# Performance work log

Measured on AMD Instinct MI355X. Metric: run time of the kernel, lower is better.

The kernel has to match this reference:

```python
import jax, jax.numpy as jnp
import numpy as np

N_NODES = 50000
N_EDGES = 600000
IN_DIM = 128
HID = 128


def gcn_conv(x, W, b, src, dst, num_nodes):
    """PyG-style GCNConv: add self-loops, symmetric D^-1/2 (A+I) D^-1/2 normalization."""
    xw = x @ W  # [N, H]
    loop = jnp.arange(num_nodes)
    s = jnp.concatenate([src, loop])
    d = jnp.concatenate([dst, loop])
    deg = jax.ops.segment_sum(jnp.ones_like(d, dtype=xw.dtype), d, num_segments=num_nodes)
    dinv = jax.lax.rsqrt(deg)  # deg >= 1 thanks to self-loops
    norm = dinv[s] * dinv[d]  # [E+N]
    msgs = xw[s] * norm[:, None]  # gather + scale, [E+N, H]
    out = jax.ops.segment_sum(msgs, d, num_segments=num_nodes)
    return out + b


def setup_inputs() -> dict:
    key = jax.random.key(0)
    ks = jax.random.split(key, 12)
    sc_in = 1.0 / np.sqrt(IN_DIM)
    sc_h = 1.0 / np.sqrt(HID)
    sc_2h = 1.0 / np.sqrt(2 * HID)
    return {
        "x": jax.random.normal(ks[0], (N_NODES, IN_DIM), jnp.float32),
        "hidden_state": jax.random.normal(ks[1], (N_NODES, HID), jnp.float32),
        "edge_index": jax.random.randint(ks[2], (2, N_EDGES), 0, N_NODES, dtype=jnp.int32),
        "W_in": jax.random.normal(ks[3], (IN_DIM, HID), jnp.float32) * sc_in,
        "b_in": jnp.zeros((HID,), jnp.float32),
        "W_hid": jax.random.normal(ks[4], (HID, HID), jnp.float32) * sc_h,
        "b_hid": jnp.zeros((HID,), jnp.float32),
        "W_z": jax.random.normal(ks[5], (2 * HID, HID), jnp.float32) * sc_2h,
        "b_z": jnp.zeros((HID,), jnp.float32),
        "W_r": jax.random.normal(ks[6], (2 * HID, HID), jnp.float32) * sc_2h,
        "b_r": jnp.zeros((HID,), jnp.float32),
        "W_c": jax.random.normal(ks[7], (2 * HID, HID), jnp.float32) * sc_2h,
        "b_c": jnp.zeros((HID,), jnp.float32),
    }


def reference(x, hidden_state, edge_index, W_in, b_in, W_hid, b_hid, W_z, b_z, W_r, b_r, W_c, b_c):
    src, dst = edge_index[0], edge_index[1]
    n = x.shape[0]
    # two stacked GCN layers (dropout identity in eval mode)
    h1 = jax.nn.relu(gcn_conv(x, W_in, b_in, src, dst, n))
    emb = gcn_conv(h1, W_hid, b_hid, src, dst, n)  # [N, H]
    # GRU-style gating
    combined = jnp.concatenate([emb, hidden_state], axis=1)  # [N, 2H]
    update = jax.nn.sigmoid(combined @ W_z + b_z)
    reset = jax.nn.sigmoid(combined @ W_r + b_r)
    cand_in = jnp.concatenate([emb, reset * hidden_state], axis=1)
    candidate = jnp.tanh(cand_in @ W_c + b_c)
    new_hidden = (1.0 - update) * hidden_state + update * candidate
    return new_hidden
```

## Files before the change

kernel.cpp:

```cpp
#include <hip/hip_runtime.h>
#include <cstdint>
#include <cstddef>

typedef unsigned short u16;
typedef unsigned int   u32;

typedef __bf16 bf8   __attribute__((ext_vector_type(8)));
typedef float  f32x4 __attribute__((ext_vector_type(4)));

__device__ __forceinline__ float b2f(u16 v) {
  union { u32 i; float f; } c; c.i = ((u32)v) << 16; return c.f;
}
__device__ __forceinline__ u16 f2b(float f) {
  union { u32 i; float f; } c; c.f = f;
  u32 x = c.i;
  u32 r = (x + 0x7FFFu + ((x >> 16) & 1u)) >> 16;
  return (u16)r;
}
__device__ __forceinline__ float sigf(float x) { return 1.0f / (1.0f + __expf(-x)); }
__device__ __forceinline__ float tanhfast(float x) { return 2.0f * sigf(2.0f * x) - 1.0f; }

__device__ __forceinline__ bf8 cvt8(const float* __restrict__ p) {
  f32x4 lo = *(const f32x4*)p;
  f32x4 hi = *(const f32x4*)(p + 4);
  union { u16 s[8]; bf8 v; } c;
#pragma unroll
  for (int i = 0; i < 4; ++i) { c.s[i] = f2b(lo[i]); c.s[4 + i] = f2b(hi[i]); }
  return c.v;
}

__device__ __forceinline__ void ld_lds16(const u16* g, u16* l) {
  __builtin_amdgcn_global_load_lds((const __attribute__((address_space(1))) void*)g,
                                   (__attribute__((address_space(3))) void*)l, 16, 0, 0);
}

#define CSR_STRIDE 80

__global__ __launch_bounds__(256) void k_transpose(
    const float* __restrict__ W0, const float* __restrict__ W1,
    const float* __restrict__ W2, const float* __restrict__ W3,
    const float* __restrict__ W4,
    u16* __restrict__ B0, u16* __restrict__ B1, u16* __restrict__ B2,
    u16* __restrict__ B3, u16* __restrict__ B4,
    int* __restrict__ cnt, int N) {
  if (blockIdx.x >= 64) {
    int i = (blockIdx.x - 64) * 256 + threadIdx.x;
    if (i < N) cnt[i] = 0;
    return;
  }
  int t = blockIdx.x * 256 + threadIdx.x;
  const float* in; u16* out; int f;
  if (t < 2048)       { in = W0; out = B0; f = t; }
  else if (t < 4096)  { in = W1; out = B1; f = t - 2048; }
  else if (t < 8192)  { in = W2; out = B2; f = t - 4096; }
  else if (t < 12288) { in = W3; out = B3; f = t - 8192; }
  else                { in = W4; out = B4; f = t - 12288; }
  int ln = f & 15, quad = (f >> 4) & 3, c = (f >> 6) & 7, ks = (f >> 9) & 3, hh = f >> 11;
  int n = c * 16 + ln;
  int k0 = hh * 128 + ks * 32 + quad * 8;
  union { u16 s[8]; uint4 q; } tmp;
#pragma unroll
  for (int j = 0; j < 8; ++j) tmp.s[j] = f2b(in[(size_t)(k0 + j) * 128 + n]);
  *(uint4*)(out + (size_t)f * 8) = tmp.q;
}

__global__ void k_fill(const int* __restrict__ src, const int* __restrict__ dst,
                       int* __restrict__ cnt, int* __restrict__ csr, int E) {
  int e = blockIdx.x * 256 + threadIdx.x;
  if (e < E) {
    int d = dst[e];
    int pos = atomicAdd(&cnt[d], 1);
    if (pos < CSR_STRIDE) csr[(size_t)d * CSR_STRIDE + pos] = src[e];
  }
}

__global__ __launch_bounds__(256) void k_agg(const u16* __restrict__ y,
                                             const int* __restrict__ cnt,
                                             const int* __restrict__ csr,
                                             const float* __restrict__ bias,
                                             u16* __restrict__ out, int relu, int N) {
  int wv = (blockIdx.x * 256 + threadIdx.x) >> 6;
  int lane = threadIdx.x & 63;
  if (wv >= N) return;
  int g = lane >> 4, t = lane & 15;
  const uint4* yq = (const uint4*)y;
  int deg = cnt[wv];
  int degc = (deg < 64) ? deg : 64;
  long base = (long)wv * CSR_STRIDE;
  int myidx = (lane < degc) ? csr[base + lane] : 0;

  float a[8];
#pragma unroll
  for (int j = 0; j < 8; ++j) a[j] = 0.0f;

  for (int b = 0; b < degc; b += 8) {
    int e0 = b + g, e1 = b + 4 + g;
    int s0 = __shfl(myidx, (e0 < degc) ? e0 : 0, 64);
    int s1 = __shfl(myidx, (e1 < degc) ? e1 : 0, 64);
    uint4 v0 = yq[(size_t)s0 * 16 + t];
    uint4 v1 = yq[(size_t)s1 * 16 + t];
    if (e0 < degc) {
      const u32* w = (const u32*)&v0;
#pragma unroll
      for (int i = 0; i < 4; ++i) { a[2*i] += b2f((u16)(w[i] & 0xFFFF)); a[2*i+1] += b2f((u16)(w[i] >> 16)); }
    }
    if (e1 < degc) {
      const u32* w = (const u32*)&v1;
#pragma unroll
      for (int i = 0; i < 4; ++i) { a[2*i] += b2f((u16)(w[i] & 0xFFFF)); a[2*i+1] += b2f((u16)(w[i] >> 16)); }
    }
  }
#pragma unroll
  for (int j = 0; j < 8; ++j) {
    a[j] += __shfl_xor(a[j], 16, 64);
    a[j] += __shfl_xor(a[j], 32, 64);
  }
  if (g == 0) {
    int degt = (deg < CSR_STRIDE) ? deg : CSR_STRIDE;
    for (int p = 64; p < degt; ++p) {
      int s = csr[base + p];
      uint4 v = yq[(size_t)s * 16 + t];
      const u32* w = (const u32*)&v;
#pragma unroll
      for (int i = 0; i < 4; ++i) { a[2*i] += b2f((u16)(w[i] & 0xFFFF)); a[2*i+1] += b2f((u16)(w[i] >> 16)); }
    }
    uint4 sv = yq[(size_t)wv * 16 + t];
    const u32* w = (const u32*)&sv;
#pragma unroll
    for (int i = 0; i < 4; ++i) { a[2*i] += b2f((u16)(w[i] & 0xFFFF)); a[2*i+1] += b2f((u16)(w[i] >> 16)); }
    float di = rsqrtf((float)deg + 1.0f);
    f32x4 b0 = *(const f32x4*)(bias + t * 8);
    f32x4 b1 = *(const f32x4*)(bias + t * 8 + 4);
    union { u16 s[8]; uint4 q; } o;
#pragma unroll
    for (int j = 0; j < 8; ++j) {
      float r = di * a[j] + ((j < 4) ? b0[j] : b1[j - 4]);
      if (relu) r = fmaxf(r, 0.0f);
      o.s[j] = f2b(r);
    }
    ((uint4*)out)[(size_t)wv * 16 + t] = o.q;
  }
}

template <bool AF>
__global__ __launch_bounds__(256) void k_gemm(
    const void* __restrict__ Av,
    const u16* __restrict__ Bt,
    const int* __restrict__ cnt,
    u16* __restrict__ outb, int M) {
  __shared__ __align__(16) u16 bs[16384];
  int tid = threadIdx.x;
  int lane = tid & 63, wave = tid >> 6;
  int ln = lane & 15, quad = lane >> 4;
  int rowbase = blockIdx.x * 64 + wave * 16;
  int rowA = rowbase + ln;
  long rA = (rowA < M) ? rowA : (M - 1);

  {
    const u16* g = Bt + wave * 4096 + lane * 8;
    u16* l = bs + wave * 4096;
#pragma unroll
    for (int i = 0; i < 8; ++i) ld_lds16(g + i * 512, l + i * 512);
  }

  bf8 af[4];
#pragma unroll
  for (int ks = 0; ks < 4; ++ks) {
    int kk = ks * 32 + quad * 8;
    if (AF) af[ks] = cvt8((const float*)Av + rA * 128 + kk);
    else    af[ks] = *(const bf8*)((const u16*)Av + rA * 128 + kk);
  }

  f32x4 acc[8];
#pragma unroll
  for (int c = 0; c < 8; ++c) { acc[c][0] = 0.f; acc[c][1] = 0.f; acc[c][2] = 0.f; acc[c][3] = 0.f; }

  __syncthreads();
#pragma unroll
  for (int ks = 0; ks < 4; ++ks) {
#pragma unroll
    for (int c = 0; c < 8; ++c) {
      bf8 bfr = *(const bf8*)(bs + ks * 4096 + c * 512 + lane * 8);
      acc[c] = __builtin_amdgcn_mfma_f32_16x16x32_bf16(af[ks], bfr, acc[c], 0, 0, 0);
    }
  }

  int rb = rowbase + quad * 4;
  float rs[4];
#pragma unroll
  for (int r = 0; r < 4; ++r) {
    int row = rb + r;
    rs[r] = (row < M) ? rsqrtf((float)cnt[row] + 1.0f) : 0.0f;
  }
#pragma unroll
  for (int c = 0; c < 8; ++c) {
    int col = c * 16 + ln;
#pragma unroll
    for (int r = 0; r < 4; ++r) {
      int row = rb + r;
      if (row < M) outb[(size_t)row * 128 + col] = f2b(acc[c][r] * rs[r]);
    }
  }
}

__global__ __launch_bounds__(256, 2) void k_gru(
    const u16* __restrict__ emb, const float* __restrict__ h,
    const u16* __restrict__ Btz, const u16* __restrict__ Btr, const u16* __restrict__ Btc,
    const float* __restrict__ bz, const float* __restrict__ br, const float* __restrict__ bc,
    float* __restrict__ out, int M) {
  __shared__ __align__(16) u16 lds[20480];
  int tid = threadIdx.x;
  int lane = tid & 63, wave = tid >> 6;
  int ln = lane & 15, quad = lane >> 4;
  int rowbase = blockIdx.x * 64 + wave * 16;
  int rowA = rowbase + ln;
  long rA = (rowA < M) ? rowA : (M - 1);
  int rb = rowbase + quad * 4;
  u16* const atw = lds + 12288 + wave * 2048;

  auto stage_zr = [&](int t, int s) {
    const u16* src = ((t & 1) ? Btr : Btz) + (t >> 1) * 4096;
#pragma unroll
    for (int i = 0; i < 2; ++i) {
      int off = (wave * 2 + i) * 512;
      ld_lds16(src + off + lane * 8, &lds[s * 4096 + off]);
    }
  };
  auto stage_c = [&](int k, int s) {
#pragma unroll
    for (int i = 0; i < 2; ++i) {
      int off = (wave * 2 + i) * 512;
      ld_lds16(Btc + k * 4096 + off + lane * 8, &lds[s * 4096 + off]);
    }
  };

  bf8 af_e[4], af_h[4];
#pragma unroll
  for (int ks = 0; ks < 4; ++ks)
    af_e[ks] = *(const bf8*)(emb + rA * 128 + ks * 32 + quad * 8);
#pragma unroll
  for (int ks = 0; ks < 4; ++ks)
    af_h[ks] = cvt8(h + rA * 128 + ks * 32 + quad * 8);

  stage_zr(0, 0);
  stage_zr(1, 1);

  f32x4 accz[8], accr[8];
#pragma unroll
  for (int c = 0; c < 8; ++c) {
    accz[c][0] = 0.f; accz[c][1] = 0.f; accz[c][2] = 0.f; accz[c][3] = 0.f;
    accr[c][0] = 0.f; accr[c][1] = 0.f; accr[c][2] = 0.f; accr[c][3] = 0.f;
  }

#pragma unroll
  for (int t = 0; t < 16; ++t) {
    if (t < 15) asm volatile("s_waitcnt vmcnt(2)\n\ts_barrier" ::: "memory");
    else        asm volatile("s_waitcnt vmcnt(0)\n\ts_barrier" ::: "memory");
    if (t < 14) stage_zr(t + 2, (t + 2) % 3);
    int ks = t >> 1;
    bf8 af = (ks < 4) ? af_e[ks] : af_h[ks - 4];
    int s = t % 3;
    f32x4* acc = (t & 1) ? accr : accz;
#pragma unroll
    for (int c = 0; c < 8; ++c) {
      bf8 bfr = *(const bf8*)(&lds[s * 4096 + (c * 64 + lane) * 8]);
      acc[c] = __builtin_amdgcn_mfma_f32_16x16x32_bf16(af, bfr, acc[c], 0, 0, 0);
    }
  }

  stage_c(0, 1);
  stage_c(1, 2);

  f32x4 hc[8];
#pragma unroll
  for (int c = 0; c < 8; ++c) {
    int col = c * 16 + ln;
#pragma unroll
    for (int r = 0; r < 4; ++r) {
      int row = rb + r;
      hc[c][r] = (row < M) ? h[(size_t)row * 128 + col] : 0.0f;
    }
  }

#pragma unroll
  for (int c = 0; c < 8; ++c) {
    int col = c * 16 + ln;
    float bzc = bz[col], brc = br[col];
#pragma unroll
    for (int r = 0; r < 4; ++r) {
      float uu = sigf(accz[c][r] + bzc);
      float rr = sigf(accr[c][r] + brc);
      accz[c][r] = uu;
      int wl = quad * 4 + r;
      int idx = (wl * 128 + col) ^ ((wl & 7) << 3);
      atw[idx] = f2b(rr * hc[c][r]);
      accr[c][r] = 0.0f;
    }
  }
  bf8 af_at[4];
#pragma unroll
  for (int ks = 0; ks < 4; ++ks) {
    int wl = ln;
    int idx = (wl * 128 + ks * 32 + quad * 8) ^ ((wl & 7) << 3);
    af_at[ks] = *(const bf8*)(&atw[idx]);
  }

#pragma unroll
  for (int j = 0; j < 8; ++j) {
    if (j < 7) asm volatile("s_waitcnt vmcnt(2)\n\ts_barrier" ::: "memory");
    else       asm volatile("s_waitcnt vmcnt(0)\n\ts_barrier" ::: "memory");
    if (j < 6) stage_c(j + 2, j % 3);
    bf8 af = (j < 4) ? af_e[j] : af_at[j - 4];
    int s = (j + 1) % 3;
#pragma unroll
    for (int c = 0; c < 8; ++c) {
      bf8 bfr = *(const bf8*)(&lds[s * 4096 + (c * 64 + lane) * 8]);
      accr[c] = __builtin_amdgcn_mfma_f32_16x16x32_bf16(af, bfr, accr[c], 0, 0, 0);
    }
  }

#pragma unroll
  for (int c = 0; c < 8; ++c) {
    int col = c * 16 + ln;
    float bcc = bc[col];
#pragma unroll
    for (int r = 0; r < 4; ++r) {
      int row = rb + r;
      if (row < M) {
        float cd = tanhfast(accr[c][r] + bcc);
        float uu = accz[c][r];
        out[(size_t)row * 128 + col] = (1.0f - uu) * hc[c][r] + uu * cd;
      }
    }
  }
}

extern "C" void kernel_launch(void* const* d_in, const int* in_sizes, int n_in,
                              void* d_out, int out_size, void* d_ws, size_t ws_size,
                              hipStream_t stream) {
  const float* x     = (const float*)d_in[0];
  const float* h     = (const float*)d_in[1];
  const int*   ei    = (const int*)d_in[2];
  const float* W_in  = (const float*)d_in[3];
  const float* b_in  = (const float*)d_in[4];
  const float* W_hid = (const float*)d_in[5];
  const float* b_hid = (const float*)d_in[6];
  const float* W_z   = (const float*)d_in[7];
  const float* b_z   = (const float*)d_in[8];
  const float* W_r   = (const float*)d_in[9];
  const float* b_r   = (const float*)d_in[10];
  const float* W_c   = (const float*)d_in[11];
  const float* b_c   = (const float*)d_in[12];

  const int N = in_sizes[0] / 128;
  const int E = in_sizes[2] / 2;
  const int* src = ei;
  const int* dst = ei + E;

  char* p = (char*)d_ws;
  auto carve = [&](size_t bytes) { char* r = p; p += (bytes + 255) & ~(size_t)255; return r; };
  u16* Bt_in   = (u16*)carve((size_t)16384 * 2);
  u16* Bt_hid  = (u16*)carve((size_t)16384 * 2);
  u16* Bt_z    = (u16*)carve((size_t)32768 * 2);
  u16* Bt_r    = (u16*)carve((size_t)32768 * 2);
  u16* Bt_c    = (u16*)carve((size_t)32768 * 2);
  int* cnt  = (int*)carve((size_t)N * 4);
  int* csr  = (int*)carve((size_t)N * CSR_STRIDE * 4);
  u16* y    = (u16*)carve((size_t)N * 128 * 2);
  u16* h1   = (u16*)carve((size_t)N * 128 * 2);
  u16* emb  = (u16*)carve((size_t)N * 128 * 2);

  int gN = (N + 255) / 256;
  int gE = (E + 255) / 256;
  int gG = (N + 63) / 64;
  int gA = (N + 3) / 4;

  k_transpose<<<64 + gN, 256, 0, stream>>>(W_in, W_hid, W_z, W_r, W_c,
                                           Bt_in, Bt_hid, Bt_z, Bt_r, Bt_c, cnt, N);
  k_fill<<<gE, 256, 0, stream>>>(src, dst, cnt, csr, E);

  k_gemm<true><<<gG, 256, 0, stream>>>(x, Bt_in, cnt, y, N);
  k_agg<<<gA, 256, 0, stream>>>(y, cnt, csr, b_in, h1, 1, N);
  k_gemm<false><<<gG, 256, 0, stream>>>(h1, Bt_hid, cnt, y, N);
  k_agg<<<gA, 256, 0, stream>>>(y, cnt, csr, b_hid, emb, 0, N);
  k_gru<<<gG, 256, 0, stream>>>(emb, h, Bt_z, Bt_r, Bt_c, b_z, b_r, b_c, (float*)d_out, N);
}
```

Before: 255.7 us.

## Restructure GRU kernel to single-wave blocks with barrier-free double-buffered staging

Turns the GRU gating kernel from 4-wave blocks, which shared each staged weight tile through a triple-buffered LDS ring with s_barrier, into one-wave blocks of 16 rows. Each wave stages the whole weight tile itself into a double buffer, using vmcnt and lgkmcnt waits instead of workgroup barriers. This removes barrier stalls and halves LDS per block, which should allow more resident blocks. In exchange, every 16-row block reloads the full weight matrices, so L2 traffic for weights is four times higher, and prefetch depth drops to one tile.

```diff
diff --git a/kernel.cpp b/kernel.cpp
--- a/kernel.cpp
+++ b/kernel.cpp
@@ -203,35 +203,28 @@
   }
 }
 
-__global__ __launch_bounds__(256, 2) void k_gru(
+__global__ __launch_bounds__(64, 2) void k_gru(
     const u16* __restrict__ emb, const float* __restrict__ h,
     const u16* __restrict__ Btz, const u16* __restrict__ Btr, const u16* __restrict__ Btc,
     const float* __restrict__ bz, const float* __restrict__ br, const float* __restrict__ bc,
     float* __restrict__ out, int M) {
-  __shared__ __align__(16) u16 lds[20480];
-  int tid = threadIdx.x;
-  int lane = tid & 63, wave = tid >> 6;
+  __shared__ __align__(16) u16 lds[10240];
+  int lane = threadIdx.x;
   int ln = lane & 15, quad = lane >> 4;
-  int rowbase = blockIdx.x * 64 + wave * 16;
+  int rowbase = blockIdx.x * 16;
   int rowA = rowbase + ln;
   long rA = (rowA < M) ? rowA : (M - 1);
   int rb = rowbase + quad * 4;
-  u16* const atw = lds + 12288 + wave * 2048;
-
-  auto stage_zr = [&](int t, int s) {
-    const u16* src = ((t & 1) ? Btr : Btz) + (t >> 1) * 4096;
-#pragma unroll
-    for (int i = 0; i < 2; ++i) {
-      int off = (wave * 2 + i) * 512;
-      ld_lds16(src + off + lane * 8, &lds[s * 4096 + off]);
-    }
+  u16* const atw = lds + 8192;
+
+  auto stage = [&](const u16* src, int s) {
+#pragma unroll
+    for (int i = 0; i < 8; ++i)
+      ld_lds16(src + i * 512 + lane * 8, &lds[s * 4096 + i * 512]);
   };
-  auto stage_c = [&](int k, int s) {
-#pragma unroll
-    for (int i = 0; i < 2; ++i) {
-      int off = (wave * 2 + i) * 512;
-      ld_lds16(Btc + k * 4096 + off + lane * 8, &lds[s * 4096 + off]);
-    }
+  auto lds_fence = [&]() {
+    asm volatile("s_waitcnt lgkmcnt(0)" ::: "memory");
+    __builtin_amdgcn_sched_barrier(0);
   };
 
   bf8 af_e[4], af_h[4];
@@ -242,8 +235,8 @@
   for (int ks = 0; ks < 4; ++ks)
     af_h[ks] = cvt8(h + rA * 128 + ks * 32 + quad * 8);
 
-  stage_zr(0, 0);
-  stage_zr(1, 1);
+  stage(Btz, 0);
+  stage(Btr, 1);
 
   f32x4 accz[8], accr[8];
 #pragma unroll
@@ -254,22 +247,26 @@
 
 #pragma unroll
   for (int t = 0; t < 16; ++t) {
-    if (t < 15) asm volatile("s_waitcnt vmcnt(2)\n\ts_barrier" ::: "memory");
-    else        asm volatile("s_waitcnt vmcnt(0)\n\ts_barrier" ::: "memory");
-    if (t < 14) stage_zr(t + 2, (t + 2) % 3);
+    asm volatile("s_waitcnt vmcnt(8)" ::: "memory");
     int ks = t >> 1;
     bf8 af = (ks < 4) ? af_e[ks] : af_h[ks - 4];
-    int s = t % 3;
+    int s = t & 1;
     f32x4* acc = (t & 1) ? accr : accz;
 #pragma unroll
     for (int c = 0; c < 8; ++c) {
       bf8 bfr = *(const bf8*)(&lds[s * 4096 + (c * 64 + lane) * 8]);
       acc[c] = __builtin_amdgcn_mfma_f32_16x16x32_bf16(af, bfr, acc[c], 0, 0, 0);
     }
-  }
-
-  stage_c(0, 1);
-  stage_c(1, 2);
+    lds_fence();
+    if (t < 14) {
+      int tn = t + 2;
+      stage(((tn & 1) ? Btr : Btz) + (tn >> 1) * 4096, tn & 1);
+    } else if (t == 14) {
+      stage(Btc, 0);
+    } else {
+      stage(Btc + 4096, 1);
+    }
+  }
 
   f32x4 hc[8];
 #pragma unroll
@@ -307,15 +304,18 @@
 
 #pragma unroll
   for (int j = 0; j < 8; ++j) {
-    if (j < 7) asm volatile("s_waitcnt vmcnt(2)\n\ts_barrier" ::: "memory");
-    else       asm volatile("s_waitcnt vmcnt(0)\n\ts_barrier" ::: "memory");
-    if (j < 6) stage_c(j + 2, j % 3);
+    if (j < 7) asm volatile("s_waitcnt vmcnt(8)" ::: "memory");
+    else       asm volatile("s_waitcnt vmcnt(0)" ::: "memory");
     bf8 af = (j < 4) ? af_e[j] : af_at[j - 4];
-    int s = (j + 1) % 3;
+    int s = j & 1;
 #pragma unroll
     for (int c = 0; c < 8; ++c) {
       bf8 bfr = *(const bf8*)(&lds[s * 4096 + (c * 64 + lane) * 8]);
       accr[c] = __builtin_amdgcn_mfma_f32_16x16x32_bf16(af, bfr, accr[c], 0, 0, 0);
+    }
+    if (j < 6) {
+      lds_fence();
+      stage(Btc + (size_t)(j + 2) * 4096, j & 1);
     }
   }
 
@@ -373,6 +373,7 @@
   int gN = (N + 255) / 256;
   int gE = (E + 255) / 256;
   int gG = (N + 63) / 64;
+  int gW = (N + 15) / 16;
   int gA = (N + 3) / 4;
 
   k_transpose<<<64 + gN, 256, 0, stream>>>(W_in, W_hid, W_z, W_r, W_c,
@@ -383,5 +384,5 @@
   k_agg<<<gA, 256, 0, stream>>>(y, cnt, csr, b_in, h1, 1, N);
   k_gemm<false><<<gG, 256, 0, stream>>>(h1, Bt_hid, cnt, y, N);
   k_agg<<<gA, 256, 0, stream>>>(y, cnt, csr, b_hid, emb, 0, N);
-  k_gru<<<gG, 256, 0, stream>>>(emb, h, Bt_z, Bt_r, Bt_c, b_z, b_r, b_c, (float*)d_out, N);
-}
+  k_gru<<<gW, 64, 0, stream>>>(emb, h, Bt_z, Bt_r, Bt_c, b_z, b_r, b_c, (float*)d_out, N);
+}
```

Measured after the change: 261.7 us. +2.3%, slower.

## Split GRU kernel columns across wave pairs with 32-row blocks

Applied to the files above, without the earlier changes.

Each GRU block now covers 32 rows instead of 64, and each pair of waves splits the 128 output columns in half, so every wave holds 4 accumulator tiles instead of 8. The reset*h tile is shared in LDS across the pair, which needs an extra barrier and lgkmcnt waits. The aim is lower register pressure, smaller LDS use and more blocks for better occupancy. The cost is reloading the weight stages for twice as many blocks and extra synchronisation.

```diff
diff --git a/kernel.cpp b/kernel.cpp
--- a/kernel.cpp
+++ b/kernel.cpp
@@ -208,15 +208,17 @@
     const u16* __restrict__ Btz, const u16* __restrict__ Btr, const u16* __restrict__ Btc,
     const float* __restrict__ bz, const float* __restrict__ br, const float* __restrict__ bc,
     float* __restrict__ out, int M) {
-  __shared__ __align__(16) u16 lds[20480];
+  __shared__ __align__(16) u16 lds[16384];
   int tid = threadIdx.x;
   int lane = tid & 63, wave = tid >> 6;
   int ln = lane & 15, quad = lane >> 4;
-  int rowbase = blockIdx.x * 64 + wave * 16;
+  int wrow  = (wave >> 1) * 16;
+  int cbase = (wave & 1) * 4;
+  int rowbase = blockIdx.x * 32 + wrow;
   int rowA = rowbase + ln;
   long rA = (rowA < M) ? rowA : (M - 1);
   int rb = rowbase + quad * 4;
-  u16* const atw = lds + 12288 + wave * 2048;
+  u16* const at = lds + 12288;
 
   auto stage_zr = [&](int t, int s) {
     const u16* src = ((t & 1) ? Btr : Btz) + (t >> 1) * 4096;
@@ -245,25 +247,25 @@
   stage_zr(0, 0);
   stage_zr(1, 1);
 
-  f32x4 accz[8], accr[8];
-#pragma unroll
-  for (int c = 0; c < 8; ++c) {
+  f32x4 accz[4], accr[4];
+#pragma unroll
+  for (int c = 0; c < 4; ++c) {
     accz[c][0] = 0.f; accz[c][1] = 0.f; accz[c][2] = 0.f; accz[c][3] = 0.f;
     accr[c][0] = 0.f; accr[c][1] = 0.f; accr[c][2] = 0.f; accr[c][3] = 0.f;
   }
 
 #pragma unroll
   for (int t = 0; t < 16; ++t) {
-    if (t < 15) asm volatile("s_waitcnt vmcnt(2)\n\ts_barrier" ::: "memory");
-    else        asm volatile("s_waitcnt vmcnt(0)\n\ts_barrier" ::: "memory");
+    if (t < 15) asm volatile("s_waitcnt vmcnt(2) lgkmcnt(0)\n\ts_barrier" ::: "memory");
+    else        asm volatile("s_waitcnt vmcnt(0) lgkmcnt(0)\n\ts_barrier" ::: "memory");
     if (t < 14) stage_zr(t + 2, (t + 2) % 3);
     int ks = t >> 1;
     bf8 af = (ks < 4) ? af_e[ks] : af_h[ks - 4];
     int s = t % 3;
     f32x4* acc = (t & 1) ? accr : accz;
 #pragma unroll
-    for (int c = 0; c < 8; ++c) {
-      bf8 bfr = *(const bf8*)(&lds[s * 4096 + (c * 64 + lane) * 8]);
+    for (int c = 0; c < 4; ++c) {
+      bf8 bfr = *(const bf8*)(&lds[s * 4096 + ((cbase + c) * 64 + lane) * 8]);
       acc[c] = __builtin_amdgcn_mfma_f32_16x16x32_bf16(af, bfr, acc[c], 0, 0, 0);
     }
   }
@@ -271,10 +273,10 @@
   stage_c(0, 1);
   stage_c(1, 2);
 
-  f32x4 hc[8];
-#pragma unroll
-  for (int c = 0; c < 8; ++c) {
-    int col = c * 16 + ln;
+  f32x4 hc[4];
+#pragma unroll
+  for (int c = 0; c < 4; ++c) {
+    int col = (cbase + c) * 16 + ln;
 #pragma unroll
     for (int r = 0; r < 4; ++r) {
       int row = rb + r;
@@ -283,45 +285,47 @@
   }
 
 #pragma unroll
-  for (int c = 0; c < 8; ++c) {
-    int col = c * 16 + ln;
+  for (int c = 0; c < 4; ++c) {
+    int col = (cbase + c) * 16 + ln;
     float bzc = bz[col], brc = br[col];
 #pragma unroll
     for (int r = 0; r < 4; ++r) {
       float uu = sigf(accz[c][r] + bzc);
       float rr = sigf(accr[c][r] + brc);
       accz[c][r] = uu;
-      int wl = quad * 4 + r;
+      int wl = wrow + quad * 4 + r;
       int idx = (wl * 128 + col) ^ ((wl & 7) << 3);
-      atw[idx] = f2b(rr * hc[c][r]);
+      at[idx] = f2b(rr * hc[c][r]);
       accr[c][r] = 0.0f;
     }
   }
+  asm volatile("s_waitcnt lgkmcnt(0)\n\ts_barrier" ::: "memory");
+
   bf8 af_at[4];
 #pragma unroll
   for (int ks = 0; ks < 4; ++ks) {
-    int wl = ln;
+    int wl = wrow + ln;
     int idx = (wl * 128 + ks * 32 + quad * 8) ^ ((wl & 7) << 3);
-    af_at[ks] = *(const bf8*)(&atw[idx]);
+    af_at[ks] = *(const bf8*)(&at[idx]);
   }
 
 #pragma unroll
   for (int j = 0; j < 8; ++j) {
-    if (j < 7) asm volatile("s_waitcnt vmcnt(2)\n\ts_barrier" ::: "memory");
-    else       asm volatile("s_waitcnt vmcnt(0)\n\ts_barrier" ::: "memory");
+    if (j < 7) asm volatile("s_waitcnt vmcnt(2) lgkmcnt(0)\n\ts_barrier" ::: "memory");
+    else       asm volatile("s_waitcnt vmcnt(0) lgkmcnt(0)\n\ts_barrier" ::: "memory");
     if (j < 6) stage_c(j + 2, j % 3);
     bf8 af = (j < 4) ? af_e[j] : af_at[j - 4];
     int s = (j + 1) % 3;
 #pragma unroll
-    for (int c = 0; c < 8; ++c) {
-      bf8 bfr = *(const bf8*)(&lds[s * 4096 + (c * 64 + lane) * 8]);
+    for (int c = 0; c < 4; ++c) {
+      bf8 bfr = *(const bf8*)(&lds[s * 4096 + ((cbase + c) * 64 + lane) * 8]);
       accr[c] = __builtin_amdgcn_mfma_f32_16x16x32_bf16(af, bfr, accr[c], 0, 0, 0);
     }
   }
 
 #pragma unroll
-  for (int c = 0; c < 8; ++c) {
-    int col = c * 16 + ln;
+  for (int c = 0; c < 4; ++c) {
+    int col = (cbase + c) * 16 + ln;
     float bcc = bc[col];
 #pragma unroll
     for (int r = 0; r < 4; ++r) {
@@ -373,6 +377,7 @@
   int gN = (N + 255) / 256;
   int gE = (E + 255) / 256;
   int gG = (N + 63) / 64;
+  int gGru = (N + 31) / 32;
   int gA = (N + 3) / 4;
 
   k_transpose<<<64 + gN, 256, 0, stream>>>(W_in, W_hid, W_z, W_r, W_c,
@@ -383,5 +388,5 @@
   k_agg<<<gA, 256, 0, stream>>>(y, cnt, csr, b_in, h1, 1, N);
   k_gemm<false><<<gG, 256, 0, stream>>>(h1, Bt_hid, cnt, y, N);
   k_agg<<<gA, 256, 0, stream>>>(y, cnt, csr, b_hid, emb, 0, N);
-  k_gru<<<gG, 256, 0, stream>>>(emb, h, Bt_z, Bt_r, Bt_c, b_z, b_r, b_c, (float*)d_out, N);
-}
+  k_gru<<<gGru, 256, 0, stream>>>(emb, h, Bt_z, Bt_r, Bt_c, b_z, b_r, b_c, (float*)d_out, N);
+}
```

Result: no change. 252.9 us (-1.1%).
